# Performance work log

Hardware: AMD Instinct MI355X
Metric: run time of the kernel (lower is better)

Reference implementation:

```python
import jax, jax.numpy as jnp
import numpy as np

# ---- fixed structural constants from the module source ----
BODY_PARTS = [[1, 2, 3], [4, 5, 6], [0, 7, 8, 9, 10], [11, 12, 13], [14, 15, 16]]
PART_EDGES = [[0, 2], [1, 2], [2, 3], [2, 4]]
N_JOINTS, N_PARTS = 17, 5
K_CHEB = 3  # ChebConv K=2 -> K+1 = 3 polynomial terms


def _pool_scatter_mats():
    # P[p, j] = 1/len(part_p) for j in part_p  (AdaptiveAvgPool1d(1) == mean)
    P = np.zeros((N_PARTS, N_JOINTS), np.float32)
    # S[j, p] = 1 if joint j belongs to part p (broadcast scatter)
    S = np.zeros((N_JOINTS, N_PARTS), np.float32)
    for p, idxs in enumerate(BODY_PARTS):
        for j in idxs:
            P[p, j] = 1.0 / len(idxs)
            S[j, p] = 1.0
    return jnp.asarray(P), jnp.asarray(S)


def _part_adj():
    # adj_mx_from_edges: symmetrize, add self loops, row-normalize
    A = np.zeros((N_PARTS, N_PARTS), np.float32)
    for i, j in PART_EDGES:
        A[i, j] = 1.0
    A = A + A.T  # edges are one-directional and disjoint -> symmetrize
    A = A + np.eye(N_PARTS, dtype=np.float32)
    A = A / A.sum(axis=1, keepdims=True)  # row-normalize
    return jnp.asarray(A)


def _cheb_basis(adj):
    # get_laplacian(normalize=True): L = I - D^{-1/2} A D^{-1/2}
    d_isqrt = jnp.sum(adj, axis=-1) ** (-0.5)
    L = jnp.eye(N_PARTS, dtype=adj.dtype) - (d_isqrt[:, None] * adj) * d_isqrt[None, :]
    I = jnp.eye(N_PARTS, dtype=adj.dtype)
    T2 = 2.0 * (L @ L) - I  # Chebyshev recurrence, K=2
    return jnp.stack([I, L, T2], axis=0)  # [3, 5, 5]


def setup_inputs() -> dict:
    key = jax.random.key(0)
    k1, k2 = jax.random.split(key)
    B, D = 8192, 512
    x = jax.random.normal(k1, (B, N_JOINTS, D), dtype=jnp.float32)
    # xavier-normal-like init for ChebConv weight [K+1, 1, in_c, out_c]
    scale = (2.0 / (D + D)) ** 0.5
    weight = jax.random.normal(k2, (K_CHEB, 1, D, D), dtype=jnp.float32) * scale
    bias = jnp.zeros((1, 1, D), dtype=jnp.float32)
    return {"x": x, "weight": weight, "bias": bias}


def reference(x, weight, bias):
    # x: [B, 17, D]; weight: [3, 1, D, D]; bias: [1, 1, D]
    P, S = _pool_scatter_mats()
    cheb = _cheb_basis(_part_adj())            # [3, 5, 5]
    part_feats = jnp.einsum('pj,bjd->bpd', P, x)              # part-wise mean pool
    prop = jnp.einsum('knm,bmd->kbnd', cheb, part_feats)      # Cheb propagation
    part_out = jnp.einsum('kbnd,kde->bne', prop, weight[:, 0]) + bias[0]  # [B, 5, D]
    return jnp.einsum('jp,bpd->bjd', S, part_out)             # broadcast to 17 joints
```

## Files before the change

### kernel.cpp

```cpp
#include <hip/hip_runtime.h>
#include <hip/hip_bf16.h>
#include <stdint.h>
#include <stddef.h>

typedef __attribute__((ext_vector_type(8))) short short8;
typedef __attribute__((ext_vector_type(4))) float f32x4;
typedef __attribute__((ext_vector_type(4))) unsigned int u32x4;

#define DIM   512
#define NJ    17
#define NPART 5
#define NB    8192
#define KDIM  1536
#define QROWS (NB*NPART)
#define ROWB  (KDIM*2)

struct Cheb { float c[3][5][5]; };

__device__ __forceinline__ void gload_lds16(const void* g, void* l) {
  __builtin_amdgcn_global_load_lds((__attribute__((address_space(1))) void*)(g),
                                   (__attribute__((address_space(3))) void*)(l),
                                   16, 0, 0);
}

__global__ __launch_bounds__(256) void pool_cheb_kernel(
    const float* __restrict__ x, __hip_bfloat16* __restrict__ Q, Cheb cb) {
  int gid = blockIdx.x * 256 + threadIdx.x;
  int b  = gid >> 7;
  int c4 = gid & 127;
  const float* xb = x + (size_t)b * (NJ * DIM) + (c4 << 2);

  f32x4 pf[5];
#pragma unroll
  for (int p = 0; p < 5; ++p) pf[p] = (f32x4){0.f, 0.f, 0.f, 0.f};

  constexpr int jpart[NJ] = {2,0,0,0,1,1,1,2,2,2,2,3,3,3,4,4,4};
#pragma unroll
  for (int j = 0; j < NJ; ++j) {
    f32x4 a = __builtin_nontemporal_load(
        reinterpret_cast<const f32x4*>(xb + j * DIM));
    pf[jpart[j]] += a;
  }
  constexpr float scl[5] = {1.f/3.f, 1.f/3.f, 0.2f, 1.f/3.f, 1.f/3.f};
#pragma unroll
  for (int p = 0; p < 5; ++p) pf[p] *= scl[p];

  char* qb = reinterpret_cast<char*>(Q);
  int cj = c4 >> 1;
#pragma unroll
  for (int k = 0; k < 3; ++k) {
#pragma unroll
    for (int n = 0; n < 5; ++n) {
      int row = b * 5 + n;
      f32x4 s = cb.c[k][n][0] * pf[0] + cb.c[k][n][1] * pf[1] +
                cb.c[k][n][2] * pf[2] + cb.c[k][n][3] * pf[3] +
                cb.c[k][n][4] * pf[4];
      alignas(8) __hip_bfloat16 o[4];
#pragma unroll
      for (int i = 0; i < 4; ++i) o[i] = __float2bfloat16(s[i]);
      int swc = (cj & 7) ^ (row & 7);
      size_t off = (size_t)row * ROWB + (size_t)(k * 8 + (cj >> 3)) * 128 +
                   (size_t)swc * 16 + (size_t)(c4 & 1) * 8;
      *reinterpret_cast<ushort4*>(qb + off) = *reinterpret_cast<const ushort4*>(o);
    }
  }
}

__global__ __launch_bounds__(256) void wt_kernel(
    const float* __restrict__ w, __hip_bfloat16* __restrict__ Wt) {
  int gid = blockIdx.x * 256 + threadIdx.x;
  int e = gid & 511;
  int chunk = gid >> 9;
  int kidx0 = chunk << 3;
  alignas(16) __hip_bfloat16 o[8];
#pragma unroll
  for (int i = 0; i < 8; ++i)
    o[i] = __float2bfloat16(w[(size_t)(kidx0 + i) * DIM + e]);
  int blk = kidx0 >> 6;
  int swc = ((kidx0 >> 3) & 7) ^ (e & 7);
  size_t off = (size_t)e * ROWB + (size_t)blk * 128 + (size_t)swc * 16;
  *reinterpret_cast<u32x4*>(reinterpret_cast<char*>(Wt) + off) =
      *reinterpret_cast<const u32x4*>(o);
}

__global__ __launch_bounds__(512) void gemm_scatter_kernel(
    const __hip_bfloat16* __restrict__ Q, const __hip_bfloat16* __restrict__ Wt,
    const float* __restrict__ bias, float* __restrict__ out) {
  __shared__ __align__(16) char LDSbuf[49152];
  char* As = LDSbuf;
  char* Bs = LDSbuf + 32768;

  int tid  = threadIdx.x;
  int lane = tid & 63;
  int wave = tid >> 6;
  int wr = wave >> 1, wc = wave & 1;
  int m0 = blockIdx.y * 256;
  int n0 = blockIdx.x * 128;

  f32x4 acc[4][4] = {};

  const char* qb = reinterpret_cast<const char*>(Q);
  const char* wb = reinterpret_cast<const char*>(Wt);
  int sr8 = lane >> 3;
  int sc  = (lane & 7) * 16;

  for (int ks = 0; ks < 24; ++ks) {
#pragma unroll
    for (int i = 0; i < 4; ++i) {
      int rbase = i * 64 + wave * 8;
      gload_lds16(qb + (size_t)(m0 + rbase + sr8) * ROWB + (size_t)ks * 128 + sc,
                  As + rbase * 128);
    }
#pragma unroll
    for (int i = 0; i < 2; ++i) {
      int rbase = i * 64 + wave * 8;
      gload_lds16(wb + (size_t)(n0 + rbase + sr8) * ROWB + (size_t)ks * 128 + sc,
                  Bs + rbase * 128);
    }
    __syncthreads();

#pragma unroll
    for (int kk = 0; kk < 2; ++kk) {
      short8 af[4], bfr[4];
#pragma unroll
      for (int mi = 0; mi < 4; ++mi) {
        int r = wr * 64 + mi * 16 + (lane & 15);
        int c7 = (kk * 4 + (lane >> 4)) ^ (r & 7);
        af[mi] = *reinterpret_cast<const short8*>(As + r * 128 + c7 * 16);
      }
#pragma unroll
      for (int ni = 0; ni < 4; ++ni) {
        int r = wc * 64 + ni * 16 + (lane & 15);
        int c7 = (kk * 4 + (lane >> 4)) ^ (r & 7);
        bfr[ni] = *reinterpret_cast<const short8*>(Bs + r * 128 + c7 * 16);
      }
#pragma unroll
      for (int mi = 0; mi < 4; ++mi)
#pragma unroll
        for (int ni = 0; ni < 4; ++ni)
          acc[mi][ni] = __builtin_amdgcn_mfma_f32_16x16x32_bf16(
              af[mi], bfr[ni], acc[mi][ni], 0, 0, 0);
    }
    __syncthreads();
  }

  int colbase = n0 + wc * 64 + (lane & 15);
  float bs[4];
#pragma unroll
  for (int ni = 0; ni < 4; ++ni) bs[ni] = bias[colbase + ni * 16];

  char* eb = LDSbuf + wave * 4352;
  int g4 = lane >> 4;
  int cc = lane & 15;

#pragma unroll
  for (int mi = 0; mi < 4; ++mi) {
#pragma unroll
    for (int ni = 0; ni < 4; ++ni)
#pragma unroll
      for (int j = 0; j < 4; ++j)
        *reinterpret_cast<float*>(
            eb + (((g4 * 4 + j) * 68 + ni * 16 + cc) << 2)) =
            acc[mi][ni][j] + bs[ni];

#pragma unroll
    for (int t = 0; t < 4; ++t) {
      u32x4 v4 = *reinterpret_cast<const u32x4*>(
          eb + ((((t * 4 + g4) * 68) + cc * 4) << 2));
      int R4 = m0 + wr * 64 + mi * 16 + t * 4 + g4;
      unsigned bb = (unsigned)R4 / 5u;
      int n = R4 - (int)bb * 5;
      unsigned mask = (n == 0) ? 0x0000Eu :
                      (n == 1) ? 0x00070u :
                      (n == 2) ? 0x00781u :
                      (n == 3) ? 0x03800u : 0x1C000u;
      float* op = out + (size_t)bb * (NJ * DIM) + (n0 + wc * 64 + cc * 4);
      while (mask) {
        int jn = __builtin_ctz(mask);
        mask &= mask - 1;
        __builtin_nontemporal_store(
            v4, reinterpret_cast<u32x4*>(op + jn * DIM));
      }
    }
  }
}

extern "C" void kernel_launch(void* const* d_in, const int* in_sizes, int n_in,
                              void* d_out, int out_size, void* d_ws, size_t ws_size,
                              hipStream_t stream) {
  const float* x    = (const float*)d_in[0];
  const float* w    = (const float*)d_in[1];
  const float* bias = (const float*)d_in[2];
  float* out = (float*)d_out;

  __hip_bfloat16* Q  = (__hip_bfloat16*)d_ws;
  __hip_bfloat16* Wt = (__hip_bfloat16*)((char*)d_ws + (size_t)QROWS * ROWB);

  Cheb cb;
  {
    double A[5][5] = {};
    const int e0[4] = {0, 1, 2, 2}, e1[4] = {2, 2, 3, 4};
    for (int t = 0; t < 4; ++t) { A[e0[t]][e1[t]] = 1.0; A[e1[t]][e0[t]] = 1.0; }
    for (int i = 0; i < 5; ++i) A[i][i] += 1.0;
    for (int i = 0; i < 5; ++i) {
      double rs = 0; for (int j = 0; j < 5; ++j) rs += A[i][j];
      for (int j = 0; j < 5; ++j) A[i][j] /= rs;
    }
    double L[5][5], T2[5][5];
    for (int i = 0; i < 5; ++i)
      for (int j = 0; j < 5; ++j) L[i][j] = (i == j ? 1.0 : 0.0) - A[i][j];
    for (int i = 0; i < 5; ++i)
      for (int j = 0; j < 5; ++j) {
        double s = 0; for (int m = 0; m < 5; ++m) s += L[i][m] * L[m][j];
        T2[i][j] = 2.0 * s - (i == j ? 1.0 : 0.0);
      }
    for (int i = 0; i < 5; ++i)
      for (int j = 0; j < 5; ++j) {
        cb.c[0][i][j] = (float)(i == j ? 1.0 : 0.0);
        cb.c[1][i][j] = (float)L[i][j];
        cb.c[2][i][j] = (float)T2[i][j];
      }
  }

  pool_cheb_kernel<<<(NB * 128) / 256, 256, 0, stream>>>(x, Q, cb);
  wt_kernel<<<(DIM * (KDIM / 8)) / 256, 256, 0, stream>>>(w, Wt);
  gemm_scatter_kernel<<<dim3(DIM / 128, QROWS / 256), 512, 0, stream>>>(Q, Wt, bias, out);
}
```

Measured before the change: 200.9 us.

## Add larger-tile double-buffered GEMM kernel with dynamic LDS and fallback

Adds a new GEMM-scatter kernel that uses a 320x256 output tile per block (5x8 MFMA tiles per wave) and double-buffers the A/B LDS stages so global-to-LDS loads for the next K step overlap compute on the current one. It needs 144 KB of dynamic LDS, which is requested with hipFuncSetAttribute, and the launch falls back to the old kernel if that call fails. The larger tile is meant to raise operand reuse and cut global traffic per flop. In exchange it needs many more accumulator registers, and it launches only 2x128 blocks, which may leave compute units underused or lower occupancy.

```diff
diff --git a/kernel.cpp b/kernel.cpp
--- a/kernel.cpp
+++ b/kernel.cpp
@@ -83,6 +83,132 @@
       *reinterpret_cast<const u32x4*>(o);
 }
 
+__global__ __launch_bounds__(512, 2) void gemm_big_kernel(
+    const __hip_bfloat16* __restrict__ Q, const __hip_bfloat16* __restrict__ Wt,
+    const float* __restrict__ bias, float* __restrict__ out) {
+  extern __shared__ __align__(16) char LDSbuf[];
+  char* As0 = LDSbuf;
+  char* As1 = LDSbuf + 40960;
+  char* Bs0 = LDSbuf + 81920;
+  char* Bs1 = LDSbuf + 114688;
+
+  int tid  = threadIdx.x;
+  int lane = tid & 63;
+  int wave = tid >> 6;
+  int wr = wave >> 1, wc = wave & 1;
+  int m0 = blockIdx.y * 320;
+  int n0 = blockIdx.x * 256;
+
+  f32x4 acc[5][8] = {};
+
+  const char* qb = reinterpret_cast<const char*>(Q);
+  const char* wb = reinterpret_cast<const char*>(Wt);
+  int sr8 = lane >> 3;
+  int sc  = (lane & 7) * 16;
+
+  const char* abase = qb + (size_t)(m0 + wave * 40 + sr8) * ROWB + sc;
+  const char* bbase = wb + (size_t)(n0 + wave * 32 + sr8) * ROWB + sc;
+  char* aldsw = (char*)0 + wave * 5120;
+  char* bldsw = (char*)0 + wave * 4096;
+
+  auto stage = [&](char* Abuf, char* Bbuf, int ks) {
+#pragma unroll
+    for (int i = 0; i < 5; ++i)
+      gload_lds16(abase + (size_t)i * (8 * ROWB) + (size_t)ks * 128,
+                  Abuf + (size_t)(aldsw - (char*)0) + i * 1024);
+#pragma unroll
+    for (int i = 0; i < 4; ++i)
+      gload_lds16(bbase + (size_t)i * (8 * ROWB) + (size_t)ks * 128,
+                  Bbuf + (size_t)(bldsw - (char*)0) + i * 1024);
+  };
+
+  auto compute = [&](const char* Abuf, const char* Bbuf) {
+#pragma unroll
+    for (int kk = 0; kk < 2; ++kk) {
+      short8 af[5];
+#pragma unroll
+      for (int mi = 0; mi < 5; ++mi) {
+        int r = wr * 80 + mi * 16 + (lane & 15);
+        int c7 = (kk * 4 + (lane >> 4)) ^ (r & 7);
+        af[mi] = *reinterpret_cast<const short8*>(Abuf + r * 128 + c7 * 16);
+      }
+#pragma unroll
+      for (int h = 0; h < 2; ++h) {
+        short8 bf[4];
+#pragma unroll
+        for (int nj = 0; nj < 4; ++nj) {
+          int r = wc * 128 + (h * 4 + nj) * 16 + (lane & 15);
+          int c7 = (kk * 4 + (lane >> 4)) ^ (r & 7);
+          bf[nj] = *reinterpret_cast<const short8*>(Bbuf + r * 128 + c7 * 16);
+        }
+#pragma unroll
+        for (int mi = 0; mi < 5; ++mi)
+#pragma unroll
+          for (int nj = 0; nj < 4; ++nj)
+            acc[mi][h * 4 + nj] = __builtin_amdgcn_mfma_f32_16x16x32_bf16(
+                af[mi], bf[nj], acc[mi][h * 4 + nj], 0, 0, 0);
+      }
+    }
+  };
+
+  stage(As0, Bs0, 0);
+  __syncthreads();
+  for (int ks = 0; ks < 22; ks += 2) {
+    stage(As1, Bs1, ks + 1);
+    compute(As0, Bs0);
+    __syncthreads();
+    stage(As0, Bs0, ks + 2);
+    compute(As1, Bs1);
+    __syncthreads();
+  }
+  stage(As1, Bs1, 23);
+  compute(As0, Bs0);
+  __syncthreads();
+  compute(As1, Bs1);
+  __syncthreads();
+
+  float bs[8];
+#pragma unroll
+  for (int ni = 0; ni < 8; ++ni)
+    bs[ni] = bias[n0 + wc * 128 + ni * 16 + (lane & 15)];
+
+  char* eb = LDSbuf + wave * 8448;
+  int halfsel = lane >> 5;
+  int col4 = lane & 31;
+
+#pragma unroll
+  for (int mi = 0; mi < 5; ++mi) {
+#pragma unroll
+    for (int ni = 0; ni < 8; ++ni)
+#pragma unroll
+      for (int j = 0; j < 4; ++j) {
+        int row = (lane >> 4) * 4 + j;
+        *reinterpret_cast<float*>(
+            eb + ((row * 132 + ni * 16 + (lane & 15)) << 2)) =
+            acc[mi][ni][j] + bs[ni];
+      }
+#pragma unroll
+    for (int rr = 0; rr < 8; ++rr) {
+      int row = rr * 2 + halfsel;
+      u32x4 v4 = *reinterpret_cast<const u32x4*>(
+          eb + ((row * 132 + col4 * 4) << 2));
+      int R = m0 + wr * 80 + mi * 16 + row;
+      unsigned bb = (unsigned)R / 5u;
+      int n = R - (int)bb * 5;
+      unsigned mask = (n == 0) ? 0x0000Eu :
+                      (n == 1) ? 0x00070u :
+                      (n == 2) ? 0x00781u :
+                      (n == 3) ? 0x03800u : 0x1C000u;
+      float* op = out + (size_t)bb * (NJ * DIM) + (n0 + wc * 128 + col4 * 4);
+      while (mask) {
+        int jn = __builtin_ctz(mask);
+        mask &= mask - 1;
+        __builtin_nontemporal_store(v4, reinterpret_cast<u32x4*>(op + jn * DIM));
+      }
+    }
+  }
+}
+
 __global__ __launch_bounds__(512) void gemm_scatter_kernel(
     const __hip_bfloat16* __restrict__ Q, const __hip_bfloat16* __restrict__ Wt,
     const float* __restrict__ bias, float* __restrict__ out) {
@@ -118,7 +244,6 @@
                   Bs + rbase * 128);
     }
     __syncthreads();
-
 #pragma unroll
     for (int kk = 0; kk < 2; ++kk) {
       short8 af[4], bfr[4];
@@ -178,8 +303,7 @@
       while (mask) {
         int jn = __builtin_ctz(mask);
         mask &= mask - 1;
-        __builtin_nontemporal_store(
-            v4, reinterpret_cast<u32x4*>(op + jn * DIM));
+        __builtin_nontemporal_store(v4, reinterpret_cast<u32x4*>(op + jn * DIM));
       }
     }
   }
@@ -224,5 +348,16 @@
 
   pool_cheb_kernel<<<(NB * 128) / 256, 256, 0, stream>>>(x, Q, cb);
   wt_kernel<<<(DIM * (KDIM / 8)) / 256, 256, 0, stream>>>(w, Wt);
-  gemm_scatter_kernel<<<dim3(DIM / 128, QROWS / 256), 512, 0, stream>>>(Q, Wt, bias, out);
-}
+
+  const int DYN_LDS = 147456;
+  hipError_t e = hipFuncSetAttribute(
+      reinterpret_cast<const void*>(gemm_big_kernel),
+      hipFuncAttributeMaxDynamicSharedMemorySize, DYN_LDS);
+  if (e == hipSuccess) {
+    gemm_big_kernel<<<dim3(DIM / 256, QROWS / 320), 512, DYN_LDS, stream>>>(
+        Q, Wt, bias, out);
+  } else {
+    gemm_scatter_kernel<<<dim3(DIM / 128, QROWS / 256), 512, 0, stream>>>(
+        Q, Wt, bias, out);
+  }
+}
```

Result: faster. 172.7 us (-14.0%).
